# Kernel tuning notes

Hardware: AMD Instinct MI355X
Metric: run time of the kernel (lower is better)

Reference implementation:

```python
import jax, jax.numpy as jnp
import numpy as np

B, S, D, H = 2, 2048, 1024, 16
DH = D // H


def _rel_shift(pos_score):
    # pos_score: [B,H,S,S] -> Transformer-XL relative shift via pad/reshape/slice
    b, h, s1, s2 = pos_score.shape
    zeros = jnp.zeros((b, h, s1, 1), dtype=pos_score.dtype)
    padded = jnp.concatenate([zeros, pos_score], axis=-1)          # [B,H,S1,S2+1]
    padded = padded.reshape(b, h, s2 + 1, s1)                       # [B,H,S2+1,S1]
    return padded[:, :, 1:].reshape(b, h, s1, s2)


def setup_inputs() -> dict:
    key = jax.random.key(0)
    ks = jax.random.split(key, 16)
    sc = 0.02
    return {
        "q": jax.random.normal(ks[0], (B, S, D), jnp.float32),
        "k": jax.random.normal(ks[1], (B, S, D), jnp.float32),
        "v": jax.random.normal(ks[2], (B, S, D), jnp.float32),
        "pos_embedding": jax.random.normal(ks[3], (B, S, D), jnp.float32),
        "Wq": jax.random.normal(ks[4], (D, D), jnp.float32) * sc,
        "bq": jnp.zeros((D,), jnp.float32),
        "Wk": jax.random.normal(ks[5], (D, D), jnp.float32) * sc,
        "bk": jnp.zeros((D,), jnp.float32),
        "Wv": jax.random.normal(ks[6], (D, D), jnp.float32) * sc,
        "bv": jnp.zeros((D,), jnp.float32),
        "Wp": jax.random.normal(ks[7], (D, D), jnp.float32) * sc,
        "u_bias": jax.random.normal(ks[8], (H, DH), jnp.float32) * sc,
        "v_bias": jax.random.normal(ks[9], (H, DH), jnp.float32) * sc,
        "Wo": jax.random.normal(ks[10], (D, D), jnp.float32) * sc,
        "bo": jnp.zeros((D,), jnp.float32),
    }


def reference(q, k, v, pos_embedding, Wq, bq, Wk, bk, Wv, bv, Wp, u_bias, v_bias, Wo, bo):
    b = q.shape[0]
    qh = (q @ Wq.T + bq).reshape(b, -1, H, DH)          # [B,S,H,dh]
    kh = (k @ Wk.T + bk).reshape(b, -1, H, DH)
    vh = (v @ Wv.T + bv).reshape(b, -1, H, DH)
    ph = (pos_embedding @ Wp.T).reshape(b, -1, H, DH)    # pos Linear has no bias
    content = jnp.einsum('bqhd,bkhd->bhqk', qh + u_bias, kh)
    pos = jnp.einsum('bqhd,bkhd->bhqk', qh + v_bias, ph)
    pos = _rel_shift(pos)
    score = (content + pos) / jnp.sqrt(jnp.float32(D))   # scaled by sqrt(d_model), as in source
    attn = jax.nn.softmax(score, axis=-1)                # dropout p=0 -> identity
    out = jnp.einsum('bhqk,bkhd->bqhd', attn, vh).reshape(b, -1, D)
    return out @ Wo.T + bo
```

## Files before the change

kernel.cpp:

```cpp
#include <hip/hip_runtime.h>

#define B_ 2
#define S_ 2048
#define D_ 1024
#define H_ 16
#define DH_ 64

typedef unsigned short u16;
typedef short v8s __attribute__((ext_vector_type(8)));
typedef float v4f __attribute__((ext_vector_type(4)));

__device__ __forceinline__ u16 f2bf(float x) {
    unsigned int u = __float_as_uint(x);
    u += 0x7fffu + ((u >> 16) & 1u);
    return (u16)(u >> 16);
}
__device__ __forceinline__ float bf2f(u16 u) {
    return __uint_as_float(((unsigned int)u) << 16);
}

typedef __attribute__((address_space(1))) void gvoid;
typedef __attribute__((address_space(3))) void lvoid;
#define CP16(g, l) __builtin_amdgcn_global_load_lds((gvoid*)(g), (lvoid*)(l), 16, 0, 0)

__global__ __launch_bounds__(256) void cvt9(
    const float* __restrict__ s0, const float* __restrict__ s1,
    const float* __restrict__ s2, const float* __restrict__ s3,
    const float* __restrict__ s4, const float* __restrict__ s5,
    const float* __restrict__ s6, const float* __restrict__ s7,
    const float* __restrict__ s8,
    u16* __restrict__ d0, u16* __restrict__ d1, u16* __restrict__ d2,
    u16* __restrict__ d3, u16* __restrict__ d4, u16* __restrict__ d5,
    u16* __restrict__ d6, u16* __restrict__ d7, u16* __restrict__ d8,
    int nbig, int nsmall)
{
    int y = blockIdx.y;
    const float* s = y==0?s0:y==1?s1:y==2?s2:y==3?s3:y==4?s4:y==5?s5:y==6?s6:y==7?s7:s8;
    u16* d = y==0?d0:y==1?d1:y==2?d2:y==3?d3:y==4?d4:y==5?d5:y==6?d6:y==7?d7:d8;
    int n4 = (y < 4) ? nbig : nsmall;
    int i = blockIdx.x * 256 + threadIdx.x;
    if (i < n4) {
        float4 v = ((const float4*)s)[i];
        ushort4 o;
        o.x = f2bf(v.x); o.y = f2bf(v.y); o.z = f2bf(v.z); o.w = f2bf(v.w);
        ((ushort4*)d)[i] = o;
    }
}

__global__ __launch_bounds__(256, 3) void gemm_proj(
    const u16* __restrict__ A0, const u16* __restrict__ A1,
    const u16* __restrict__ A2, const u16* __restrict__ A3,
    const u16* __restrict__ W0, const u16* __restrict__ W1,
    const u16* __restrict__ W2, const u16* __restrict__ W3,
    const float* __restrict__ b0, const float* __restrict__ b1,
    const float* __restrict__ b2,
    u16* __restrict__ C0, u16* __restrict__ C1,
    u16* __restrict__ VT, u16* __restrict__ C3)
{
    const int K = D_, N = D_;
    const int proj = blockIdx.z;
    const u16* A = proj==0?A0:proj==1?A1:proj==2?A2:A3;
    const u16* W = proj==0?W0:proj==1?W1:proj==2?W2:W3;
    const float* bias = proj==0?b0:proj==1?b1:proj==2?b2:nullptr;

    __shared__ u16 As[128 * 32];
    __shared__ u16 Ws[128 * 32];
    const int tid  = threadIdx.x;
    const int wave = tid >> 6, lane = tid & 63;
    const int quad = lane >> 4, l15 = lane & 15;
    const int m0 = blockIdx.y * 128, n0 = blockIdx.x * 128;
    const int srow = lane >> 2, scol = (lane & 3) * 8;
    const int wr = wave >> 1, wc = wave & 1;

    v4f acc[4][4];
    #pragma unroll
    for (int i = 0; i < 4; ++i)
        #pragma unroll
        for (int j = 0; j < 4; ++j) acc[i][j] = (v4f){0.f, 0.f, 0.f, 0.f};

    for (int kb = 0; kb < K; kb += 32) {
        __syncthreads();
        #pragma unroll
        for (int c2 = 0; c2 < 2; ++c2) {
            int c = wave * 2 + c2;
            CP16(A + (size_t)(m0 + c * 16 + srow) * K + kb + scol, &As[c * 512]);
            CP16(W + (size_t)(n0 + c * 16 + srow) * K + kb + scol, &Ws[c * 512]);
        }
        __syncthreads();
        v8s af[4], bf[4];
        #pragma unroll
        for (int i = 0; i < 4; ++i)
            af[i] = *(const v8s*)&As[(wr * 64 + i * 16 + l15) * 32 + quad * 8];
        #pragma unroll
        for (int j = 0; j < 4; ++j)
            bf[j] = *(const v8s*)&Ws[(wc * 64 + j * 16 + l15) * 32 + quad * 8];
        #pragma unroll
        for (int i = 0; i < 4; ++i)
            #pragma unroll
            for (int j = 0; j < 4; ++j)
                acc[i][j] = __builtin_amdgcn_mfma_f32_16x16x32_bf16(af[i], bf[j], acc[i][j], 0, 0, 0);
    }

    float bb[4];
    #pragma unroll
    for (int j = 0; j < 4; ++j)
        bb[j] = bias ? bias[n0 + wc * 64 + j * 16 + l15] : 0.f;

    if (proj == 2) {
        #pragma unroll
        for (int i = 0; i < 4; ++i)
            #pragma unroll
            for (int j = 0; j < 4; ++j) {
                int r0 = m0 + wr * 64 + i * 16 + quad * 4;
                int c  = n0 + wc * 64 + j * 16 + l15;
                ushort4 pw;
                pw.x = f2bf(acc[i][j][0] + bb[j]);
                pw.y = f2bf(acc[i][j][1] + bb[j]);
                pw.z = f2bf(acc[i][j][2] + bb[j]);
                pw.w = f2bf(acc[i][j][3] + bb[j]);
                size_t row_vt = (size_t)((r0 >> 11) * 16 + (c >> 6)) * 64 + (c & 63);
                *(ushort4*)&VT[row_vt * S_ + (r0 & 2047)] = pw;
            }
    } else {
        u16* C = proj == 0 ? C0 : proj == 1 ? C1 : C3;
        #pragma unroll
        for (int i = 0; i < 4; ++i)
            #pragma unroll
            for (int j = 0; j < 4; ++j)
                #pragma unroll
                for (int reg = 0; reg < 4; ++reg) {
                    int r = m0 + wr * 64 + i * 16 + quad * 4 + reg;
                    int c = n0 + wc * 64 + j * 16 + l15;
                    C[(size_t)r * N + c] = f2bf(acc[i][j][reg] + bb[j]);
                }
    }
}

__global__ __launch_bounds__(256, 3) void gemm_out(
    const u16* __restrict__ A, const u16* __restrict__ W,
    const float* __restrict__ bias, float* __restrict__ C)
{
    const int K = D_, N = D_;
    __shared__ u16 As[64 * 32];
    __shared__ u16 Ws[128 * 32];
    const int tid  = threadIdx.x;
    const int wave = tid >> 6, lane = tid & 63;
    const int quad = lane >> 4, l15 = lane & 15;
    const int m0 = blockIdx.y * 64, n0 = blockIdx.x * 128;
    const int srow = lane >> 2, scol = (lane & 3) * 8;
    const int wr = wave >> 1, wc = wave & 1;

    v4f acc[2][4];
    #pragma unroll
    for (int i = 0; i < 2; ++i)
        #pragma unroll
        for (int j = 0; j < 4; ++j) acc[i][j] = (v4f){0.f, 0.f, 0.f, 0.f};

    for (int kb = 0; kb < K; kb += 32) {
        __syncthreads();
        CP16(A + (size_t)(m0 + wave * 16 + srow) * K + kb + scol, &As[wave * 512]);
        CP16(W + (size_t)(n0 + wave * 16 + srow) * K + kb + scol, &Ws[wave * 512]);
        CP16(W + (size_t)(n0 + (wave + 4) * 16 + srow) * K + kb + scol, &Ws[(wave + 4) * 512]);
        __syncthreads();
        v8s af[2], bf[4];
        #pragma unroll
        for (int i = 0; i < 2; ++i)
            af[i] = *(const v8s*)&As[(wr * 32 + i * 16 + l15) * 32 + quad * 8];
        #pragma unroll
        for (int j = 0; j < 4; ++j)
            bf[j] = *(const v8s*)&Ws[(wc * 64 + j * 16 + l15) * 32 + quad * 8];
        #pragma unroll
        for (int i = 0; i < 2; ++i)
            #pragma unroll
            for (int j = 0; j < 4; ++j)
                acc[i][j] = __builtin_amdgcn_mfma_f32_16x16x32_bf16(af[i], bf[j], acc[i][j], 0, 0, 0);
    }

    #pragma unroll
    for (int i = 0; i < 2; ++i)
        #pragma unroll
        for (int j = 0; j < 4; ++j)
            #pragma unroll
            for (int reg = 0; reg < 4; ++reg) {
                int r = m0 + wr * 32 + i * 16 + quad * 4 + reg;
                int c = n0 + wc * 64 + j * 16 + l15;
                C[(size_t)r * N + c] = acc[i][j][reg] + bias[c];
            }
}

__global__ __launch_bounds__(256)
__attribute__((amdgpu_waves_per_eu(4, 4)))
void rel_attn12(
    const u16* __restrict__ QH, const u16* __restrict__ KH,
    const u16* __restrict__ VT, const u16* __restrict__ PH,
    const float* __restrict__ ub, const float* __restrict__ vb,
    u16* __restrict__ AO)
{
    __shared__ u16 Ks[64 * 64];
    __shared__ u16 VTs[64 * 64];
    __shared__ u16 PmT[4][80][20];
    __shared__ u16 ps[4][16][72];

    const int tid  = threadIdx.x;
    const int wave = tid >> 6, lane = tid & 63;
    const int quad = lane >> 4, l15 = lane & 15;

    const int wg  = blockIdx.x + 32 * blockIdx.y;
    const int xcd = wg & 7;
    const int i2  = wg >> 3;
    const int bh  = xcd + 8 * (i2 & 3);
    const int xt  = i2 >> 2;

    const int q0 = (xt * 4 + wave) * 16;
    const int bb = bh >> 4, h = bh & 15;
    const size_t base = (size_t)bb * S_ * D_ + (size_t)h * DH_;
    const size_t vtb  = (size_t)bh * DH_ * S_;

    const int lr8 = lane >> 3;
    const int lc8 = ((lane & 7) ^ lr8) * 8;
    const int ksw = (l15 & 7) * 8;

    v8s quf[2], qvf0[2], qvf1[2];
    #pragma unroll
    for (int kc = 0; kc < 2; ++kc) {
        int r0 = q0 + l15;
        int r1 = min(r0 + 1, S_ - 1);
        v8s raw0 = *(const v8s*)&QH[base + (size_t)r0 * D_ + kc * 32 + quad * 8];
        v8s raw1 = *(const v8s*)&QH[base + (size_t)r1 * D_ + kc * 32 + quad * 8];
        #pragma unroll
        for (int j = 0; j < 8; ++j) {
            float ubj = ub[h * DH_ + kc * 32 + quad * 8 + j];
            float vbj = vb[h * DH_ + kc * 32 + quad * 8 + j];
            float f0 = bf2f((u16)raw0[j]);
            quf[kc][j]  = (short)f2bf(f0 + ubj);
            qvf0[kc][j] = (short)f2bf(f0 + vbj);
            qvf1[kc][j] = (short)f2bf(bf2f((u16)raw1[j]) + vbj);
        }
    }

    v4f o[4];
    float l_r[4];
    #pragma unroll
    for (int i = 0; i < 4; ++i) { o[i] = (v4f){0.f, 0.f, 0.f, 0.f}; l_r[i] = 0.f; }

    const int wb = l15 - quad * 4 + 15;

    auto body = [&](int k0, const int phase) {
        __syncthreads();

        #pragma unroll
        for (int c = 0; c < 2; ++c) {
            int seg = wave * 2 + c;
            CP16(KH + base + (size_t)(k0 + seg * 8 + lr8) * D_ + lc8, &Ks[seg * 512]);
            CP16(VT + vtb + (size_t)(seg * 8 + lr8) * S_ + k0 + lc8, &VTs[seg * 512]);
        }

        const int tmin = k0 - q0 - 15;
        const int jbase = (phase == 0) ? (S_ - 1 + tmin) : (tmin - 2);

        auto phaddr = [&](int wcl) -> const u16* {
            int rw = wcl * 16 + l15;
            int j;
            if (phase == 1) {
                int t = tmin + rw;
                j = (t <= 0) ? (S_ - 1 + t) : max(t - 2, 0);
            } else {
                j = jbase + rw;
            }
            return &PH[base + (size_t)j * D_ + quad * 8];
        };

        {
            const u16* ph0 = phaddr(0);
            v8s p0 = *(const v8s*)ph0;
            v8s p1 = *(const v8s*)(ph0 + 32);
            const bool doA = (tmin <= 0);
            #pragma unroll
            for (int wcl = 0; wcl < 5; ++wcl) {
                v8s n0, n1;
                if (wcl < 4) {
                    const u16* phn = phaddr(wcl + 1);
                    n0 = *(const v8s*)phn;
                    n1 = *(const v8s*)(phn + 32);
                }
                int rw = wcl * 16 + l15;
                v4f sel;
                if (phase == 1) {
                    int t = tmin + rw;
                    v4f a1 = (v4f){0.f, 0.f, 0.f, 0.f};
                    a1 = __builtin_amdgcn_mfma_f32_16x16x32_bf16(qvf1[0], p0, a1, 0, 0, 0);
                    a1 = __builtin_amdgcn_mfma_f32_16x16x32_bf16(qvf1[1], p1, a1, 0, 0, 0);
                    sel = a1;
                    if (doA) {
                        v4f a0 = (v4f){0.f, 0.f, 0.f, 0.f};
                        a0 = __builtin_amdgcn_mfma_f32_16x16x32_bf16(qvf0[0], p0, a0, 0, 0, 0);
                        a0 = __builtin_amdgcn_mfma_f32_16x16x32_bf16(qvf0[1], p1, a0, 0, 0, 0);
                        sel = (t >= 2) ? a1 : a0;
                    }
                } else {
                    const v8s a0s = (phase == 0) ? qvf0[0] : qvf1[0];
                    const v8s a1s = (phase == 0) ? qvf0[1] : qvf1[1];
                    v4f a = (v4f){0.f, 0.f, 0.f, 0.f};
                    a = __builtin_amdgcn_mfma_f32_16x16x32_bf16(a0s, p0, a, 0, 0, 0);
                    a = __builtin_amdgcn_mfma_f32_16x16x32_bf16(a1s, p1, a, 0, 0, 0);
                    sel = a;
                }
                ushort4 pw;
                pw.x = f2bf(sel[0]); pw.y = f2bf(sel[1]); pw.z = f2bf(sel[2]); pw.w = f2bf(sel[3]);
                *(ushort4*)&PmT[wave][rw][quad * 4] = pw;
                p0 = n0; p1 = n1;
            }
        }

        __syncthreads();

        #pragma unroll
        for (int ct = 0; ct < 4; ++ct) {
            int kr = (ct * 16 + l15) * 64;
            v8s kbf0 = *(const v8s*)&Ks[kr + ((quad * 8) ^ ksw)];
            v8s kbf1 = *(const v8s*)&Ks[kr + ((32 + quad * 8) ^ ksw)];
            v4f cs = (v4f){0.f, 0.f, 0.f, 0.f};
            cs = __builtin_amdgcn_mfma_f32_16x16x32_bf16(quf[0], kbf0, cs, 0, 0, 0);
            cs = __builtin_amdgcn_mfma_f32_16x16x32_bf16(quf[1], kbf1, cs, 0, 0, 0);
            #pragma unroll
            for (int reg = 0; reg < 4; ++reg) {
                int qrow = quad * 4 + reg;
                int wcol = ct * 16 + wb - reg;
                float pos = bf2f(PmT[wave][wcol][qrow]);
                if (phase == 1) {
                    int t = tmin + wcol;
                    if (t == 1) pos = 0.f;
                }
                float e = __expf((cs[reg] + pos) * 0.03125f);
                ps[wave][qrow][ct * 16 + l15] = f2bf(e);
                l_r[reg] += e;
            }
        }

        v8s af0 = *(const v8s*)&ps[wave][l15][quad * 8];
        v8s af1 = *(const v8s*)&ps[wave][l15][32 + quad * 8];
        #pragma unroll
        for (int dt = 0; dt < 4; ++dt) {
            int vr = (dt * 16 + l15) * 64;
            v8s vbf0 = *(const v8s*)&VTs[vr + ((quad * 8) ^ ksw)];
            v8s vbf1 = *(const v8s*)&VTs[vr + ((32 + quad * 8) ^ ksw)];
            o[dt] = __builtin_amdgcn_mfma_f32_16x16x32_bf16(af0, vbf0, o[dt], 0, 0, 0);
            o[dt] = __builtin_amdgcn_mfma_f32_16x16x32_bf16(af1, vbf1, o[dt], 0, 0, 0);
        }
    };

    const int k1end   = (q0 >= 63) ? ((((q0 - 63) >> 6) + 1) << 6) : 0;
    const int k2start = min((((q0 + 80) >> 6) << 6), S_);

    int k0 = 0;
    for (; k0 < k1end; k0 += 64)   body(k0, 0);
    for (; k0 < k2start; k0 += 64) body(k0, 1);
    for (; k0 < S_; k0 += 64)      body(k0, 2);

    #pragma unroll
    for (int reg = 0; reg < 4; ++reg) {
        float s = l_r[reg];
        #pragma unroll
        for (int off = 1; off < 16; off <<= 1)
            s += __shfl_xor(s, off, 16);
        l_r[reg] = 1.f / s;
    }
    #pragma unroll
    for (int dt = 0; dt < 4; ++dt)
        #pragma unroll
        for (int reg = 0; reg < 4; ++reg)
            AO[base + (size_t)(q0 + quad * 4 + reg) * D_ + dt * 16 + l15] =
                f2bf(o[dt][reg] * l_r[reg]);
}

extern "C" void kernel_launch(void* const* d_in, const int* in_sizes, int n_in,
                              void* d_out, int out_size, void* d_ws, size_t ws_size,
                              hipStream_t stream)
{
    (void)in_sizes; (void)n_in; (void)out_size; (void)ws_size;
    const float* q   = (const float*)d_in[0];
    const float* k   = (const float*)d_in[1];
    const float* v   = (const float*)d_in[2];
    const float* pe  = (const float*)d_in[3];
    const float* Wq  = (const float*)d_in[4];
    const float* bq  = (const float*)d_in[5];
    const float* Wk  = (const float*)d_in[6];
    const float* bk  = (const float*)d_in[7];
    const float* Wv  = (const float*)d_in[8];
    const float* bv  = (const float*)d_in[9];
    const float* Wp  = (const float*)d_in[10];
    const float* ub  = (const float*)d_in[11];
    const float* vbs = (const float*)d_in[12];
    const float* Wo  = (const float*)d_in[13];
    const float* bo  = (const float*)d_in[14];
    float* out = (float*)d_out;

    const size_t NSD = (size_t)B_ * S_ * D_;
    const size_t DD  = (size_t)D_ * D_;
    u16* ws = (u16*)d_ws;
    u16* qB  = ws;
    u16* kB  = qB + NSD;
    u16* vB  = kB + NSD;
    u16* pB  = vB + NSD;
    u16* WqB = pB + NSD;
    u16* WkB = WqB + DD;
    u16* WvB = WkB + DD;
    u16* WpB = WvB + DD;
    u16* WoB = WpB + DD;
    u16* QH  = WoB + DD;
    u16* KH  = QH + NSD;
    u16* VT  = KH + NSD;
    u16* PHb = VT + NSD;
    u16* AO  = qB;

    const int M = B_ * S_;

    cvt9<<<dim3((int)(NSD / 4 / 256), 9), 256, 0, stream>>>(
        q, k, v, pe, Wq, Wk, Wv, Wp, Wo,
        qB, kB, vB, pB, WqB, WkB, WvB, WpB, WoB,
        (int)(NSD / 4), (int)(DD / 4));

    gemm_proj<<<dim3(D_ / 128, M / 128, 4), 256, 0, stream>>>(
        qB, kB, vB, pB, WqB, WkB, WvB, WpB, bq, bk, bv, QH, KH, VT, PHb);

    rel_attn12<<<dim3(S_ / 64, B_ * H_), 256, 0, stream>>>(QH, KH, VT, PHb, ub, vbs, AO);

    gemm_out<<<dim3(D_ / 128, M / 64), 256, 0, stream>>>(AO, WoB, bo, out);
}
```

Baseline: 392.5 us.

## Deepen projection GEMM K-tile with swizzled LDS and split attention softmax-PV into halves

The projection GEMM now stages 64-wide K tiles instead of 32, using an XOR-swizzled LDS layout. This halves the number of barrier pairs per K sweep and is meant to avoid LDS bank conflicts on the fragment reads. In the attention kernel the score/exp/PV loop is split into two 32-column halves, so the probability staging buffer shrinks and each half feeds the PV MFMAs sooner. The PmT padding is also reduced, which lowers LDS use but may bring back bank conflicts on the transposed position reads.

Measured after the change: 396.6 us. No clear change (+1.0%).

```diff
diff --git a/kernel.cpp b/kernel.cpp
--- a/kernel.cpp
+++ b/kernel.cpp
@@ -63,42 +63,48 @@
     const u16* W = proj==0?W0:proj==1?W1:proj==2?W2:W3;
     const float* bias = proj==0?b0:proj==1?b1:proj==2?b2:nullptr;
 
-    __shared__ u16 As[128 * 32];
-    __shared__ u16 Ws[128 * 32];
+    __shared__ u16 As[128 * 64];
+    __shared__ u16 Ws[128 * 64];
     const int tid  = threadIdx.x;
     const int wave = tid >> 6, lane = tid & 63;
     const int quad = lane >> 4, l15 = lane & 15;
     const int m0 = blockIdx.y * 128, n0 = blockIdx.x * 128;
-    const int srow = lane >> 2, scol = (lane & 3) * 8;
     const int wr = wave >> 1, wc = wave & 1;
 
+    const int lr8 = lane >> 3;
+    const int lc8 = ((lane & 7) ^ lr8) * 8;
+    const int ksw = (l15 & 7) * 8;
+
     v4f acc[4][4];
     #pragma unroll
     for (int i = 0; i < 4; ++i)
         #pragma unroll
         for (int j = 0; j < 4; ++j) acc[i][j] = (v4f){0.f, 0.f, 0.f, 0.f};
 
-    for (int kb = 0; kb < K; kb += 32) {
-        __syncthreads();
-        #pragma unroll
-        for (int c2 = 0; c2 < 2; ++c2) {
-            int c = wave * 2 + c2;
-            CP16(A + (size_t)(m0 + c * 16 + srow) * K + kb + scol, &As[c * 512]);
-            CP16(W + (size_t)(n0 + c * 16 + srow) * K + kb + scol, &Ws[c * 512]);
-        }
-        __syncthreads();
-        v8s af[4], bf[4];
-        #pragma unroll
-        for (int i = 0; i < 4; ++i)
-            af[i] = *(const v8s*)&As[(wr * 64 + i * 16 + l15) * 32 + quad * 8];
-        #pragma unroll
-        for (int j = 0; j < 4; ++j)
-            bf[j] = *(const v8s*)&Ws[(wc * 64 + j * 16 + l15) * 32 + quad * 8];
-        #pragma unroll
-        for (int i = 0; i < 4; ++i)
+    for (int kb = 0; kb < K; kb += 64) {
+        __syncthreads();
+        #pragma unroll
+        for (int c = 0; c < 4; ++c) {
+            int seg = wave * 4 + c;
+            CP16(A + (size_t)(m0 + seg * 8 + lr8) * K + kb + lc8, &As[seg * 512]);
+            CP16(W + (size_t)(n0 + seg * 8 + lr8) * K + kb + lc8, &Ws[seg * 512]);
+        }
+        __syncthreads();
+        #pragma unroll
+        for (int kk = 0; kk < 2; ++kk) {
+            v8s af[4], bf[4];
+            #pragma unroll
+            for (int i = 0; i < 4; ++i)
+                af[i] = *(const v8s*)&As[(wr * 64 + i * 16 + l15) * 64 + ((kk * 32 + quad * 8) ^ ksw)];
             #pragma unroll
             for (int j = 0; j < 4; ++j)
-                acc[i][j] = __builtin_amdgcn_mfma_f32_16x16x32_bf16(af[i], bf[j], acc[i][j], 0, 0, 0);
+                bf[j] = *(const v8s*)&Ws[(wc * 64 + j * 16 + l15) * 64 + ((kk * 32 + quad * 8) ^ ksw)];
+            #pragma unroll
+            for (int i = 0; i < 4; ++i)
+                #pragma unroll
+                for (int j = 0; j < 4; ++j)
+                    acc[i][j] = __builtin_amdgcn_mfma_f32_16x16x32_bf16(af[i], bf[j], acc[i][j], 0, 0, 0);
+        }
     }
 
     float bb[4];
@@ -190,7 +196,7 @@
 
 __global__ __launch_bounds__(256)
 __attribute__((amdgpu_waves_per_eu(4, 4)))
-void rel_attn12(
+void rel_attn13(
     const u16* __restrict__ QH, const u16* __restrict__ KH,
     const u16* __restrict__ VT, const u16* __restrict__ PH,
     const float* __restrict__ ub, const float* __restrict__ vb,
@@ -198,8 +204,8 @@
 {
     __shared__ u16 Ks[64 * 64];
     __shared__ u16 VTs[64 * 64];
-    __shared__ u16 PmT[4][80][20];
-    __shared__ u16 ps[4][16][72];
+    __shared__ u16 PmT[4][80][16];
+    __shared__ u16 ps[4][16][40];
 
     const int tid  = threadIdx.x;
     const int wave = tid >> 6, lane = tid & 63;
@@ -315,37 +321,37 @@
         __syncthreads();
 
         #pragma unroll
-        for (int ct = 0; ct < 4; ++ct) {
-            int kr = (ct * 16 + l15) * 64;
-            v8s kbf0 = *(const v8s*)&Ks[kr + ((quad * 8) ^ ksw)];
-            v8s kbf1 = *(const v8s*)&Ks[kr + ((32 + quad * 8) ^ ksw)];
-            v4f cs = (v4f){0.f, 0.f, 0.f, 0.f};
-            cs = __builtin_amdgcn_mfma_f32_16x16x32_bf16(quf[0], kbf0, cs, 0, 0, 0);
-            cs = __builtin_amdgcn_mfma_f32_16x16x32_bf16(quf[1], kbf1, cs, 0, 0, 0);
-            #pragma unroll
-            for (int reg = 0; reg < 4; ++reg) {
-                int qrow = quad * 4 + reg;
-                int wcol = ct * 16 + wb - reg;
-                float pos = bf2f(PmT[wave][wcol][qrow]);
-                if (phase == 1) {
-                    int t = tmin + wcol;
-                    if (t == 1) pos = 0.f;
+        for (int hf = 0; hf < 2; ++hf) {
+            #pragma unroll
+            for (int c2 = 0; c2 < 2; ++c2) {
+                int ct = hf * 2 + c2;
+                int kr = (ct * 16 + l15) * 64;
+                v8s kbf0 = *(const v8s*)&Ks[kr + ((quad * 8) ^ ksw)];
+                v8s kbf1 = *(const v8s*)&Ks[kr + ((32 + quad * 8) ^ ksw)];
+                v4f cs = (v4f){0.f, 0.f, 0.f, 0.f};
+                cs = __builtin_amdgcn_mfma_f32_16x16x32_bf16(quf[0], kbf0, cs, 0, 0, 0);
+                cs = __builtin_amdgcn_mfma_f32_16x16x32_bf16(quf[1], kbf1, cs, 0, 0, 0);
+                #pragma unroll
+                for (int reg = 0; reg < 4; ++reg) {
+                    int qrow = quad * 4 + reg;
+                    int wcol = ct * 16 + wb - reg;
+                    float pos = bf2f(PmT[wave][wcol][qrow]);
+                    if (phase == 1) {
+                        int t = tmin + wcol;
+                        if (t == 1) pos = 0.f;
+                    }
+                    float e = __expf((cs[reg] + pos) * 0.03125f);
+                    ps[wave][qrow][c2 * 16 + l15] = f2bf(e);
+                    l_r[reg] += e;
                 }
-                float e = __expf((cs[reg] + pos) * 0.03125f);
-                ps[wave][qrow][ct * 16 + l15] = f2bf(e);
-                l_r[reg] += e;
-            }
-        }
-
-        v8s af0 = *(const v8s*)&ps[wave][l15][quad * 8];
-        v8s af1 = *(const v8s*)&ps[wave][l15][32 + quad * 8];
-        #pragma unroll
-        for (int dt = 0; dt < 4; ++dt) {
-            int vr = (dt * 16 + l15) * 64;
-            v8s vbf0 = *(const v8s*)&VTs[vr + ((quad * 8) ^ ksw)];
-            v8s vbf1 = *(const v8s*)&VTs[vr + ((32 + quad * 8) ^ ksw)];
-            o[dt] = __builtin_amdgcn_mfma_f32_16x16x32_bf16(af0, vbf0, o[dt], 0, 0, 0);
-            o[dt] = __builtin_amdgcn_mfma_f32_16x16x32_bf16(af1, vbf1, o[dt], 0, 0, 0);
+            }
+            v8s af = *(const v8s*)&ps[wave][l15][quad * 8];
+            #pragma unroll
+            for (int dt = 0; dt < 4; ++dt) {
+                int vr = (dt * 16 + l15) * 64;
+                v8s vbf = *(const v8s*)&VTs[vr + ((hf * 32 + quad * 8) ^ ksw)];
+                o[dt] = __builtin_amdgcn_mfma_f32_16x16x32_bf16(af, vbf, o[dt], 0, 0, 0);
+            }
         }
     };
 
@@ -423,7 +429,7 @@
     gemm_proj<<<dim3(D_ / 128, M / 128, 4), 256, 0, stream>>>(
         qB, kB, vB, pB, WqB, WkB, WvB, WpB, bq, bk, bv, QH, KH, VT, PHb);
 
-    rel_attn12<<<dim3(S_ / 64, B_ * H_), 256, 0, stream>>>(QH, KH, VT, PHb, ub, vbs, AO);
+    rel_attn13<<<dim3(S_ / 64, B_ * H_), 256, 0, stream>>>(QH, KH, VT, PHb, ub, vbs, AO);
 
     gemm_out<<<dim3(D_ / 128, M / 64), 256, 0, stream>>>(AO, WoB, bo, out);
 }
```
